# Performance work log

Measured on AMD Instinct MI355X. Metric: run time of the kernel, lower is better.

The kernel has to match this reference:

```python
import jax, jax.numpy as jnp
import numpy as np

N_USERS = 100000
N_ENTITY = 100000
D = 64
N_RK = 3
B = 16384
LA = 20   # authors per user
LC = 5    # genres per user


def setup_inputs() -> dict:
    key = jax.random.key(0)
    ks = jax.random.split(key, 6)
    return {
        "user_id": jax.random.randint(ks[0], (B,), 0, N_USERS),
        "artists_id": jax.random.randint(ks[1], (B, LA), 0, N_ENTITY),
        "categories_id": jax.random.randint(ks[2], (B, LC), 0, N_ENTITY),
        "rate": 0,  # dropout prob; eval mode -> identity
        "user_factors": jax.random.normal(ks[3], (N_USERS, D), jnp.float32),
        "entity_factors": jax.random.normal(ks[4], (N_ENTITY, D), jnp.float32),
        "relation_k": jax.random.normal(ks[5], (D, N_RK), jnp.float32),
    }


def _contrib(idx, users, entity_factors):
    # idx: [B, L] entity indices; users: [B, D]
    emb = entity_factors[idx]                      # [B, L, D] gather
    pre = jnp.einsum("bld,bd->bl", emb, users)     # per-aspect mat-vec (niubi)
    return pre.mean(axis=1), pre                   # mean over segment -> [B]


def reference(user_id, artists_id, categories_id, rate, user_factors,
              entity_factors, relation_k):
    users = user_factors[user_id]                               # [B, D]
    # importance of each aspect type
    scores = jax.nn.softmax(
        jax.nn.leaky_relu(users @ relation_k, negative_slope=0.2), axis=1)  # [B, 3]
    s_act = scores[:, 0]
    s_dir = scores[:, 1]
    # contribution of each aspect (ragged gather-matvec-mean, vectorized)
    c_act, niubi_act = _contrib(artists_id, users, entity_factors)
    c_dir, niubi_dir = _contrib(categories_id, users, entity_factors)
    importance_sum = s_act + s_dir
    prediction = (c_act * s_act + c_dir * s_dir) / importance_sum
    return prediction, scores, c_act, c_dir, niubi_act, niubi_dir
```

## Files before the change

### kernel.cpp

```cpp
#include <hip/hip_runtime.h>

constexpr int B  = 16384;
constexpr int D  = 64;
constexpr int LA = 20;
constexpr int LC = 5;

__device__ __forceinline__ float waveReduceSum(float v) {
    #pragma unroll
    for (int off = 32; off >= 1; off >>= 1)
        v += __shfl_xor(v, off, 64);
    return v;
}

__global__ __launch_bounds__(256, 4) void aspect_kernel(
    const int*   __restrict__ user_id,
    const int*   __restrict__ artists_id,
    const int*   __restrict__ categories_id,
    const float* __restrict__ user_factors,
    const float* __restrict__ entity_factors,
    const float* __restrict__ relation_k,
    float*       __restrict__ out)
{
    const int lane = threadIdx.x & 63;
    const int wid  = threadIdx.x >> 6;
    const int b    = (blockIdx.x << 2) + wid;
    if (b >= B) return;

    float* pred    = out;
    float* scores  = out + B;
    float* c_act_o = out + B + 3 * B;
    float* c_dir_o = out + B + 4 * B;
    float* niubiA  = out + B + 5 * B;
    float* niubiC  = niubiA + (size_t)B * LA;

    const int   uid = user_id[b];
    const float u   = user_factors[(size_t)uid * D + lane];

    float p0 = u * relation_k[lane * 3 + 0];
    float p1 = u * relation_k[lane * 3 + 1];
    float p2 = u * relation_k[lane * 3 + 2];
    #pragma unroll
    for (int off = 32; off >= 1; off >>= 1) {
        p0 += __shfl_xor(p0, off, 64);
        p1 += __shfl_xor(p1, off, 64);
        p2 += __shfl_xor(p2, off, 64);
    }
    p0 = p0 >= 0.f ? p0 : 0.2f * p0;
    p1 = p1 >= 0.f ? p1 : 0.2f * p1;
    p2 = p2 >= 0.f ? p2 : 0.2f * p2;
    const float m   = fmaxf(p0, fmaxf(p1, p2));
    const float e0  = expf(p0 - m), e1 = expf(p1 - m), e2 = expf(p2 - m);
    const float inv = 1.f / (e0 + e1 + e2);
    const float s0 = e0 * inv, s1 = e1 * inv, s2 = e2 * inv;

    float sumA = 0.f, nvA = 0.f;
    #pragma unroll
    for (int l = 0; l < LA; ++l) {
        const int idx = artists_id[b * LA + l];
        const float pre = waveReduceSum(entity_factors[(size_t)idx * D + lane] * u);
        sumA += pre;
        if (lane == l) nvA = pre;
    }
    const float c_act = sumA * (1.f / LA);

    float sumC = 0.f, nvC = 0.f;
    #pragma unroll
    for (int l = 0; l < LC; ++l) {
        const int idx = categories_id[b * LC + l];
        const float pre = waveReduceSum(entity_factors[(size_t)idx * D + lane] * u);
        sumC += pre;
        if (lane == l) nvC = pre;
    }
    const float c_dir = sumC * (1.f / LC);

    if (lane < LA) niubiA[(size_t)b * LA + lane] = nvA;
    if (lane < LC) niubiC[(size_t)b * LC + lane] = nvC;
    if (lane < 3)  scores[b * 3 + lane] = (lane == 0) ? s0 : (lane == 1 ? s1 : s2);
    if (lane == 0) {
        pred[b]    = (c_act * s0 + c_dir * s1) / (s0 + s1);
        c_act_o[b] = c_act;
        c_dir_o[b] = c_dir;
    }
}

extern "C" void kernel_launch(void* const* d_in, const int* in_sizes, int n_in,
                              void* d_out, int out_size, void* d_ws, size_t ws_size,
                              hipStream_t stream) {
    const int*   user_id        = (const int*)d_in[0];
    const int*   artists_id     = (const int*)d_in[1];
    const int*   categories_id  = (const int*)d_in[2];
    const float* user_factors   = (const float*)d_in[4];
    const float* entity_factors = (const float*)d_in[5];
    const float* relation_k     = (const float*)d_in[6];
    float*       out            = (float*)d_out;

    const int waves_per_block = 4;
    const int grid = B / waves_per_block;
    aspect_kernel<<<grid, 64 * waves_per_block, 0, stream>>>(
        user_id, artists_id, categories_id, user_factors, entity_factors, relation_k, out);
}
```

Baseline: 120.2 us.

## Map each row to 16 lanes with float4 gathers and batched swizzle reductions

Each batch row now gets a 16-lane group instead of a full 64-lane wave. Every lane loads a float4 slice of the entity and user vectors. The per-entity dot products are batched into register arrays and reduced with ds_swizzle butterflies over 16 lanes, which replaces a serialized 6-step shuffle reduction per entity. Outputs are written with vectorized float4 stores. This cuts shuffle traffic and increases memory-level parallelism, at the cost of higher register pressure from the 20-element arrays and a fast __expf approximation.

```diff
diff --git a/kernel.cpp b/kernel.cpp
--- a/kernel.cpp
+++ b/kernel.cpp
@@ -5,11 +5,21 @@
 constexpr int LA = 20;
 constexpr int LC = 5;
 
-__device__ __forceinline__ float waveReduceSum(float v) {
+template <int PAT>
+__device__ __forceinline__ float swz(float v) {
+    return __int_as_float(__builtin_amdgcn_ds_swizzle(__float_as_int(v), PAT));
+}
+
+template <int N>
+__device__ __forceinline__ void reduce16(float (&p)[N]) {
     #pragma unroll
-    for (int off = 32; off >= 1; off >>= 1)
-        v += __shfl_xor(v, off, 64);
-    return v;
+    for (int l = 0; l < N; ++l) p[l] += swz<0x201F>(p[l]);
+    #pragma unroll
+    for (int l = 0; l < N; ++l) p[l] += swz<0x101F>(p[l]);
+    #pragma unroll
+    for (int l = 0; l < N; ++l) p[l] += swz<0x081F>(p[l]);
+    #pragma unroll
+    for (int l = 0; l < N; ++l) p[l] += swz<0x041F>(p[l]);
 }
 
 __global__ __launch_bounds__(256, 4) void aspect_kernel(
@@ -21,62 +31,83 @@
     const float* __restrict__ relation_k,
     float*       __restrict__ out)
 {
-    const int lane = threadIdx.x & 63;
-    const int wid  = threadIdx.x >> 6;
-    const int b    = (blockIdx.x << 2) + wid;
-    if (b >= B) return;
+    const int tid = threadIdx.x;
+    const int sl  = tid & 15;
+    const int grp = tid >> 4;
+    const int b   = (blockIdx.x << 4) + grp;
 
     float* pred    = out;
     float* scores  = out + B;
-    float* c_act_o = out + B + 3 * B;
-    float* c_dir_o = out + B + 4 * B;
-    float* niubiA  = out + B + 5 * B;
+    float* c_act_o = out + (size_t)4 * B;
+    float* c_dir_o = out + (size_t)5 * B;
+    float* niubiA  = out + (size_t)6 * B;
     float* niubiC  = niubiA + (size_t)B * LA;
 
-    const int   uid = user_id[b];
-    const float u   = user_factors[(size_t)uid * D + lane];
+    const int    uid = user_id[b];
+    const float4 u4  = *(const float4*)&user_factors[(size_t)uid * D + sl * 4];
 
-    float p0 = u * relation_k[lane * 3 + 0];
-    float p1 = u * relation_k[lane * 3 + 1];
-    float p2 = u * relation_k[lane * 3 + 2];
-    #pragma unroll
-    for (int off = 32; off >= 1; off >>= 1) {
-        p0 += __shfl_xor(p0, off, 64);
-        p1 += __shfl_xor(p1, off, 64);
-        p2 += __shfl_xor(p2, off, 64);
+    float ps[3] = {0.f, 0.f, 0.f};
+    {
+        const int d0 = sl * 4;
+        ps[0] = fmaf(u4.x, relation_k[(d0+0)*3+0], fmaf(u4.y, relation_k[(d0+1)*3+0],
+                fmaf(u4.z, relation_k[(d0+2)*3+0], u4.w * relation_k[(d0+3)*3+0])));
+        ps[1] = fmaf(u4.x, relation_k[(d0+0)*3+1], fmaf(u4.y, relation_k[(d0+1)*3+1],
+                fmaf(u4.z, relation_k[(d0+2)*3+1], u4.w * relation_k[(d0+3)*3+1])));
+        ps[2] = fmaf(u4.x, relation_k[(d0+0)*3+2], fmaf(u4.y, relation_k[(d0+1)*3+2],
+                fmaf(u4.z, relation_k[(d0+2)*3+2], u4.w * relation_k[(d0+3)*3+2])));
     }
-    p0 = p0 >= 0.f ? p0 : 0.2f * p0;
-    p1 = p1 >= 0.f ? p1 : 0.2f * p1;
-    p2 = p2 >= 0.f ? p2 : 0.2f * p2;
-    const float m   = fmaxf(p0, fmaxf(p1, p2));
-    const float e0  = expf(p0 - m), e1 = expf(p1 - m), e2 = expf(p2 - m);
+    reduce16(ps);
+    float q0 = ps[0] >= 0.f ? ps[0] : 0.2f * ps[0];
+    float q1 = ps[1] >= 0.f ? ps[1] : 0.2f * ps[1];
+    float q2 = ps[2] >= 0.f ? ps[2] : 0.2f * ps[2];
+    const float m   = fmaxf(q0, fmaxf(q1, q2));
+    const float e0  = __expf(q0 - m), e1 = __expf(q1 - m), e2 = __expf(q2 - m);
     const float inv = 1.f / (e0 + e1 + e2);
     const float s0 = e0 * inv, s1 = e1 * inv, s2 = e2 * inv;
 
-    float sumA = 0.f, nvA = 0.f;
+    float pa[LA];
     #pragma unroll
     for (int l = 0; l < LA; ++l) {
-        const int idx = artists_id[b * LA + l];
-        const float pre = waveReduceSum(entity_factors[(size_t)idx * D + lane] * u);
-        sumA += pre;
-        if (lane == l) nvA = pre;
+        const int    idx = artists_id[b * LA + l];
+        const float4 e   = *(const float4*)&entity_factors[(size_t)idx * D + sl * 4];
+        pa[l] = fmaf(e.x, u4.x, fmaf(e.y, u4.y, fmaf(e.z, u4.z, e.w * u4.w)));
     }
+    reduce16(pa);
+    float sumA = 0.f;
+    #pragma unroll
+    for (int l = 0; l < LA; ++l) sumA += pa[l];
     const float c_act = sumA * (1.f / LA);
 
-    float sumC = 0.f, nvC = 0.f;
+    float pc[LC];
     #pragma unroll
     for (int l = 0; l < LC; ++l) {
-        const int idx = categories_id[b * LC + l];
-        const float pre = waveReduceSum(entity_factors[(size_t)idx * D + lane] * u);
-        sumC += pre;
-        if (lane == l) nvC = pre;
+        const int    idx = categories_id[b * LC + l];
+        const float4 e   = *(const float4*)&entity_factors[(size_t)idx * D + sl * 4];
+        pc[l] = fmaf(e.x, u4.x, fmaf(e.y, u4.y, fmaf(e.z, u4.z, e.w * u4.w)));
     }
+    reduce16(pc);
+    float sumC = 0.f;
+    #pragma unroll
+    for (int l = 0; l < LC; ++l) sumC += pc[l];
     const float c_dir = sumC * (1.f / LC);
 
-    if (lane < LA) niubiA[(size_t)b * LA + lane] = nvA;
-    if (lane < LC) niubiC[(size_t)b * LC + lane] = nvC;
-    if (lane < 3)  scores[b * 3 + lane] = (lane == 0) ? s0 : (lane == 1 ? s1 : s2);
-    if (lane == 0) {
+    if (sl < 5) {
+        float4 v;
+        v.x = sl == 0 ? pa[0] : sl == 1 ? pa[4]  : sl == 2 ? pa[8]  : sl == 3 ? pa[12] : pa[16];
+        v.y = sl == 0 ? pa[1] : sl == 1 ? pa[5]  : sl == 2 ? pa[9]  : sl == 3 ? pa[13] : pa[17];
+        v.z = sl == 0 ? pa[2] : sl == 1 ? pa[6]  : sl == 2 ? pa[10] : sl == 3 ? pa[14] : pa[18];
+        v.w = sl == 0 ? pa[3] : sl == 1 ? pa[7]  : sl == 2 ? pa[11] : sl == 3 ? pa[15] : pa[19];
+        *(float4*)&niubiA[(size_t)b * LA + sl * 4] = v;
+    }
+    if (sl < LC) {
+        const float v = sl == 0 ? pc[0] : sl == 1 ? pc[1] : sl == 2 ? pc[2] : sl == 3 ? pc[3] : pc[4];
+        niubiC[(size_t)b * LC + sl] = v;
+    }
+    if (sl < 3) {
+        const float v = sl == 0 ? s0 : sl == 1 ? s1 : s2;
+        scores[b * 3 + sl] = v;
+    }
+    if (sl == 0) {
         pred[b]    = (c_act * s0 + c_dir * s1) / (s0 + s1);
         c_act_o[b] = c_act;
         c_dir_o[b] = c_dir;
@@ -94,8 +125,8 @@
     const float* relation_k     = (const float*)d_in[6];
     float*       out            = (float*)d_out;
 
-    const int waves_per_block = 4;
-    const int grid = B / waves_per_block;
-    aspect_kernel<<<grid, 64 * waves_per_block, 0, stream>>>(
+    const int rows_per_block = 16;
+    const int grid = B / rows_per_block;
+    aspect_kernel<<<grid, 256, 0, stream>>>(
         user_id, artists_id, categories_id, user_factors, entity_factors, relation_k, out);
 }
```

Result: faster. 104.9 us (-12.7%).
